# Kernel tuning notes

Measured on AMD Instinct MI355X. Metric: run time of the kernel, lower is better.

The kernel has to match this reference:

```python
import jax, jax.numpy as jnp
import numpy as np

EMBED_DIM = 1024
CONTEXT_LEN = 2048
NUM_HEADS = 16
HEAD_DIM = EMBED_DIM // NUM_HEADS
BATCH = 2
SEQ = 2048


def setup_inputs() -> dict:
    key = jax.random.key(0)
    ks = jax.random.split(key, 6)
    s = 1.0 / np.sqrt(EMBED_DIM)
    x = jax.random.normal(ks[0], (BATCH, SEQ, EMBED_DIM), dtype=jnp.float32)
    # nn.Linear weights stored as [out, in]; we keep [in, out] for x @ W
    W_q = jax.random.uniform(ks[1], (EMBED_DIM, EMBED_DIM), jnp.float32, -s, s)
    W_k = jax.random.uniform(ks[2], (EMBED_DIM, EMBED_DIM), jnp.float32, -s, s)
    W_v = jax.random.uniform(ks[3], (EMBED_DIM, EMBED_DIM), jnp.float32, -s, s)
    W_o = jax.random.uniform(ks[4], (EMBED_DIM, EMBED_DIM), jnp.float32, -s, s)
    b_o = jax.random.uniform(ks[5], (EMBED_DIM,), jnp.float32, -s, s)
    return {"x": x, "W_q": W_q, "W_k": W_k, "W_v": W_v, "W_o": W_o, "b_o": b_o}


def reference(x, W_q, W_k, W_v, W_o, b_o):
    b, s, _ = x.shape
    # project and split heads: [b, s, e] -> [b, h, s, d]
    def heads(t):
        return t.reshape(b, s, NUM_HEADS, HEAD_DIM).transpose(0, 2, 1, 3)
    q = heads(x @ W_q)
    k = heads(x @ W_k)
    v = heads(x @ W_v)
    scores = jnp.einsum("bhqd,bhkd->bhqk", q, k)  # full seq x seq scores
    causal = jnp.triu(jnp.ones((s, s), dtype=bool), k=1)
    scores = jnp.where(causal, -jnp.inf, scores)
    attn = jax.nn.softmax(scores / np.sqrt(HEAD_DIM).astype(np.float32), axis=-1)
    ctx = jnp.einsum("bhqk,bhkd->bhqd", attn, v)
    ctx = ctx.transpose(0, 2, 1, 3).reshape(b, s, EMBED_DIM)
    return ctx @ W_o + b_o
```

## Files before the change

kernel.cpp:

```cpp
#include <hip/hip_runtime.h>

#define EMBED 1024
#define SEQL  2048
#define NHEAD 16
#define HDIM  64
#define NBATCH 2
#define MROWS 4096

typedef __attribute__((ext_vector_type(4))) float  f32x4;
typedef __attribute__((ext_vector_type(8))) __bf16 bf16x8;

__device__ __forceinline__ short f2bf(float f){
  __bf16 h = (__bf16)f;
  union { __bf16 h; short s; } u; u.h = h;
  return u.s;
}

#define GLDS(gp, lp) __builtin_amdgcn_global_load_lds( \
    (const __attribute__((address_space(1))) void*)(gp), \
    (__attribute__((address_space(3))) void*)(lp), 16, 0, 0)

__global__ __launch_bounds__(256) void prep_kernel(const float* __restrict__ x,
    const float* __restrict__ W0, const float* __restrict__ W1,
    const float* __restrict__ W2, const float* __restrict__ W3,
    short* __restrict__ Xb, short* __restrict__ WtAll){
  const int z = blockIdx.z;
  if (z < 4){
    __shared__ float T[64][65];
    const int idx = blockIdx.y*32 + blockIdx.x;
    if (idx >= 256) return;
    const float* W = (z==0)?W0:(z==1)?W1:(z==2)?W2:W3;
    short* Wt = WtAll + z*(EMBED*EMBED);
    const int bx = (idx & 15)*64;
    const int by = (idx >> 4)*64;
    const int c4 = (threadIdx.x & 15)*4;
    const int tr = threadIdx.x >> 4;
    #pragma unroll
    for (int i=0;i<4;++i){
      int r = 16*i + tr;
      float4 v = *(const float4*)(W + (by + r)*EMBED + bx + c4);
      T[c4+0][r] = v.x; T[c4+1][r] = v.y; T[c4+2][r] = v.z; T[c4+3][r] = v.w;
    }
    __syncthreads();
    #pragma unroll
    for (int i=0;i<4;++i){
      int n = 16*i + tr;
      short4 o;
      o.x = f2bf(T[n][c4+0]); o.y = f2bf(T[n][c4+1]);
      o.z = f2bf(T[n][c4+2]); o.w = f2bf(T[n][c4+3]);
      *(short4*)(Wt + (bx + n)*EMBED + by + c4) = o;
    }
  } else {
    const int blk = (z-4)*1024 + blockIdx.y*32 + blockIdx.x;
    const int i = (blk*256 + threadIdx.x)*4;
    float4 v = *(const float4*)(x + i);
    short4 o; o.x=f2bf(v.x); o.y=f2bf(v.y); o.z=f2bf(v.z); o.w=f2bf(v.w);
    *(short4*)(Xb + i) = o;
  }
}

__device__ __forceinline__ void gemm_tile_128(const short* __restrict__ A,
    const short* __restrict__ Bt, short* As, short* Bs, int m0, int n0, f32x4 acc[4][4]){
  const int tid  = threadIdx.x;
  const int lane = tid & 63;
  const int wid  = tid >> 6;
  const int wrow = (wid >> 1) * 64, wcol = (wid & 1) * 64;
  const int arow = tid >> 2, acol8 = (tid & 3) * 8;
  const int l15 = lane & 15, lg = lane >> 4;

  auto STAGE = [&](int b, int k0){
    short* as = As + b*4096;
    short* bs = Bs + b*4096;
    GLDS(A  + (m0      + arow) * 1024 + k0 + acol8, as + tid*8);
    GLDS(A  + (m0 + 64 + arow) * 1024 + k0 + acol8, as + 2048 + tid*8);
    GLDS(Bt + (n0      + arow) * 1024 + k0 + acol8, bs + tid*8);
    GLDS(Bt + (n0 + 64 + arow) * 1024 + k0 + acol8, bs + 2048 + tid*8);
  };

  auto KSTEP = [&](int b){
    const short* as = As + b*4096;
    const short* bs = Bs + b*4096;
    bf16x8 a[4], bb[4];
    #pragma unroll
    for (int i=0;i<4;++i) a[i]  = *(const bf16x8*)(as + (wrow+16*i+l15)*32 + 8*lg);
    #pragma unroll
    for (int j=0;j<4;++j) bb[j] = *(const bf16x8*)(bs + (wcol+16*j+l15)*32 + 8*lg);
    #pragma unroll
    for (int i=0;i<4;++i)
      #pragma unroll
      for (int j=0;j<4;++j)
        acc[i][j] = __builtin_amdgcn_mfma_f32_16x16x32_bf16(a[i], bb[j], acc[i][j], 0,0,0);
  };

  STAGE(0, 0); STAGE(1, 32);
  __syncthreads();
  for (int p = 0; p < 16; ++p){
    const int k0 = p*64;
    if (p + 1 < 16){ STAGE((2*p+2)&3, k0+64); STAGE((2*p+3)&3, k0+96); }
    KSTEP((2*p)&3);
    KSTEP((2*p+1)&3);
    __syncthreads();
  }
}

__device__ __forceinline__ void gemm_tile_64(const short* __restrict__ A,
    const short* __restrict__ Bt, short* As, short* Bs, int m0, int n0, f32x4 acc[2][4]){
  const int tid  = threadIdx.x;
  const int lane = tid & 63;
  const int wid  = tid >> 6;
  const int wrow = (wid >> 1) * 32, wcol = (wid & 1) * 64;
  const int arow = tid >> 2, acol8 = (tid & 3) * 8;
  const int l15 = lane & 15, lg = lane >> 4;

  auto STAGE = [&](int b, int k0){
    short* as = As + b*2048;
    short* bs = Bs + b*4096;
    GLDS(A  + (m0      + arow) * 1024 + k0 + acol8, as + tid*8);
    GLDS(Bt + (n0      + arow) * 1024 + k0 + acol8, bs + tid*8);
    GLDS(Bt + (n0 + 64 + arow) * 1024 + k0 + acol8, bs + 2048 + tid*8);
  };

  auto KSTEP = [&](int b){
    const short* as = As + b*2048;
    const short* bs = Bs + b*4096;
    bf16x8 a[2], bb[4];
    #pragma unroll
    for (int i=0;i<2;++i) a[i]  = *(const bf16x8*)(as + (wrow+16*i+l15)*32 + 8*lg);
    #pragma unroll
    for (int j=0;j<4;++j) bb[j] = *(const bf16x8*)(bs + (wcol+16*j+l15)*32 + 8*lg);
    #pragma unroll
    for (int i=0;i<2;++i)
      #pragma unroll
      for (int j=0;j<4;++j)
        acc[i][j] = __builtin_amdgcn_mfma_f32_16x16x32_bf16(a[i], bb[j], acc[i][j], 0,0,0);
  };

  STAGE(0, 0); STAGE(1, 32);
  __syncthreads();
  for (int p = 0; p < 16; ++p){
    const int k0 = p*64;
    if (p + 1 < 16){ STAGE((2*p+2)&3, k0+64); STAGE((2*p+3)&3, k0+96); }
    KSTEP((2*p)&3);
    KSTEP((2*p+1)&3);
    __syncthreads();
  }
}

__global__ __launch_bounds__(256) void gemm_qkv_kernel(const short* __restrict__ Xb,
    const short* __restrict__ WtAll, short* __restrict__ Q, short* __restrict__ K,
    short* __restrict__ Vt){
  __shared__ __align__(16) short SH[32768];
  short* As = SH;
  short* Bs = SH + 16384;
  const int m0 = blockIdx.x*128, n0 = blockIdx.y*128, z = blockIdx.z;
  const short* Bt = WtAll + z*(EMBED*EMBED);
  f32x4 acc[4][4] = {};
  gemm_tile_128(Xb, Bt, As, Bs, m0, n0, acc);
  const int tid  = threadIdx.x;
  const int lane = tid & 63;
  const int wid  = tid >> 6;
  const int wrow = (wid >> 1) * 64, wcol = (wid & 1) * 64;
  const int l15 = lane & 15, lg = lane >> 4;
  const int bb = m0 >> 11, srow0 = m0 & 2047;

  if (z < 2){
    short* out = z ? K : Q;
    const float qscl = (z==0) ? (0.125f * 1.44269504f) : 1.0f;
    #pragma unroll
    for (int i=0;i<4;++i)
      #pragma unroll
      for (int j=0;j<4;++j)
        #pragma unroll
        for (int r=0;r<4;++r){
          int m = m0 + wrow + 16*i + 4*lg + r;
          int n = n0 + wcol + 16*j + l15;
          int srow = m & 2047, hh = n >> 6, d = n & 63;
          out[(((bb<<4)+hh)*SEQL + srow)*HDIM + d] = f2bf(acc[i][j][r] * qscl);
        }
  } else {
    short* T = SH;
    #pragma unroll
    for (int i=0;i<4;++i)
      #pragma unroll
      for (int j=0;j<4;++j){
        int n_loc = wcol + 16*j + l15;
        int mb    = wrow + 16*i + 4*lg;
        short4 pk;
        pk.x = f2bf(acc[i][j][0]); pk.y = f2bf(acc[i][j][1]);
        pk.z = f2bf(acc[i][j][2]); pk.w = f2bf(acc[i][j][3]);
        *(short4*)(T + n_loc*128 + (mb ^ ((n_loc & 7) << 3))) = pk;
      }
    __syncthreads();
    #pragma unroll
    for (int it=0; it<8; ++it){
      int n_loc = 16*it + (tid >> 4);
      int mch   = (tid & 15) * 8;
      int4 v = *(const int4*)(T + n_loc*128 + (mch ^ ((n_loc & 7) << 3)));
      int n_glob = n0 + n_loc;
      int hh = n_glob >> 6, d = n_glob & 63;
      *(int4*)(Vt + (((bb<<4)+hh)*HDIM + d)*SEQL + srow0 + mch) = v;
    }
  }
}

__global__ __launch_bounds__(256) void gemm_out_kernel(const short* __restrict__ Ctx,
    const short* __restrict__ WtO, const float* __restrict__ bias, float* __restrict__ out){
  __shared__ __align__(16) short As[4*2048], Bs[4*4096];
  const int m0 = blockIdx.x*64, n0 = blockIdx.y*128;
  f32x4 acc[2][4] = {};
  gemm_tile_64(Ctx, WtO, As, Bs, m0, n0, acc);
  const int lane = threadIdx.x & 63;
  const int wid  = threadIdx.x >> 6;
  const int wrow = (wid >> 1) * 32, wcol = (wid & 1) * 64;
  const int l15 = lane & 15, lg = lane >> 4;
  #pragma unroll
  for (int i=0;i<2;++i)
    #pragma unroll
    for (int j=0;j<4;++j)
      #pragma unroll
      for (int r=0;r<4;++r){
        int m = m0 + wrow + 16*i + 4*lg + r;
        int n = n0 + wcol + 16*j + l15;
        out[m*EMBED + n] = acc[i][j][r] + bias[n];
      }
}

__global__ __launch_bounds__(512, 4) void attn_kernel(const short* __restrict__ Q,
    const short* __restrict__ K, const short* __restrict__ Vt, short* __restrict__ Ctx){
  __shared__ __align__(16) char lds[81920];
  const int tid  = threadIdx.x;
  const int lane = tid & 63;
  const int wid  = tid >> 6;
  const int bid   = blockIdx.x;
  const int xcd   = bid & 7;
  const int i7    = bid >> 3;
  const int bh    = xcd + 8*(i7 & 3);
  const int cidx  = i7 >> 2;
  const int chunk = (cidx < 8) ? cidx : 23 - cidx;
  const int q0blk = chunk * 128;
  const int ntp   = chunk + 1;
  const int q0w   = q0blk + 16*wid;
  const int qlast = q0w + 15;

  const short* Qh  = Q  + bh*(SEQL*HDIM);
  const char*  KhB = (const char*)(K  + bh*(SEQL*HDIM));
  const char*  VhB = (const char*)(Vt + bh*(HDIM*SEQL));
  const int l15 = lane & 15, lg = lane >> 4;
  const int lg20 = 20 * lg;
  const int swE = (l15 & 7) << 3;
  const int swB = (l15 & 7) << 4;
  const int laneRow = lane >> 3;
  const int colSwz  = 16 * ((lane & 7) ^ laneRow);
  const int r0 = 8 * wid;

  const short* qp = Qh + (q0w + l15)*HDIM + 8*lg;
  bf16x8 bq0 = *(const bf16x8*)qp;
  bf16x8 bq1 = *(const bf16x8*)(qp + 32);

  f32x4 acc[4];
  #pragma unroll
  for (int j=0; j<4; ++j) acc[j] = (f32x4){0.f,0.f,0.f,0.f};
  float mrun = -3e30f, lrun = 0.f;

  short* pw = (short*)(lds + 65536 + wid*2048);

  auto STAGE = [&](int b, int t){
    char* kb = lds + b*16384;
    char* vb = kb + 8192;
    const int kv0 = t*64;
    GLDS(KhB + (kv0 + r0 + laneRow)*128 + colSwz, kb + r0*128);
    GLDS(VhB + (r0 + laneRow)*4096 + kv0*2 + colSwz, vb + r0*128);
  };

  auto QKHALF = [&](const char* kb, f32x4 sc[4]){
    #pragma unroll
    for (int c=0; c<4; ++c){
      const char* kr = kb + (16*c + l15)*128;
      bf16x8 k0 = *(const bf16x8*)(kr + ((16*lg) ^ swB));
      bf16x8 k1 = *(const bf16x8*)(kr + ((64 + 16*lg) ^ swB));
      f32x4 z = (f32x4){0.f,0.f,0.f,0.f};
      z = __builtin_amdgcn_mfma_f32_16x16x32_bf16(k0, bq0, z, 0,0,0);
      z = __builtin_amdgcn_mfma_f32_16x16x32_bf16(k1, bq1, z, 0,0,0);
      sc[c] = z;
    }
  };

  STAGE(0, 0); STAGE(1, 1);
  __syncthreads();

  for (int tp = 0; tp < ntp; ++tp){
    const int t0   = 2*tp;
    const int kv00 = t0*64;
    const int kv01 = kv00 + 64;
    if (tp + 1 < ntp){ STAGE((t0+2)&3, t0+2); STAGE((t0+3)&3, t0+3); }
    if (kv00 <= qlast){
      const char* kb0 = lds + (t0&3)*16384;
      const char* kb1 = lds + ((t0+1)&3)*16384;
      const bool  h1  = (kv01 <= qlast);
      f32x4 sc0[4], sc1[4];
      __builtin_amdgcn_s_setprio(1);
      QKHALF(kb0, sc0);
      if (h1) QKHALF(kb1, sc1);
      __builtin_amdgcn_s_setprio(0);
      if (kv00 + 63 > q0w){
        #pragma unroll
        for (int c=0; c<4; ++c)
          #pragma unroll
          for (int r=0; r<4; ++r)
            if (kv00 + 16*c + 4*lg + r > q0w + l15) sc0[c][r] = -3e30f;
      }
      if (h1 && kv01 + 63 > q0w){
        #pragma unroll
        for (int c=0; c<4; ++c)
          #pragma unroll
          for (int r=0; r<4; ++r)
            if (kv01 + 16*c + 4*lg + r > q0w + l15) sc1[c][r] = -3e30f;
      }
      float cm[4];
      #pragma unroll
      for (int c=0; c<4; ++c)
        cm[c] = fmaxf(fmaxf(sc0[c][0], sc0[c][1]), fmaxf(sc0[c][2], sc0[c][3]));
      float pm = fmaxf(fmaxf(cm[0], cm[1]), fmaxf(cm[2], cm[3]));
      if (h1){
        float dm[4];
        #pragma unroll
        for (int c=0; c<4; ++c)
          dm[c] = fmaxf(fmaxf(sc1[c][0], sc1[c][1]), fmaxf(sc1[c][2], sc1[c][3]));
        pm = fmaxf(pm, fmaxf(fmaxf(dm[0], dm[1]), fmaxf(dm[2], dm[3])));
      }
      pm = fmaxf(pm, __shfl_xor(pm, 16));
      pm = fmaxf(pm, __shfl_xor(pm, 32));
      const int resc = !__all(pm <= mrun);
      float mn = mrun, ss = 1.0f;
      if (resc){
        mn = fmaxf(mrun, pm);
        ss = __builtin_amdgcn_exp2f(mrun - mn);
        mrun = mn;
      }
      #pragma unroll
      for (int c=0; c<4; ++c)
        #pragma unroll
        for (int r=0; r<4; ++r)
          sc0[c][r] = __builtin_amdgcn_exp2f(sc0[c][r] - mn);
      float cs[4];
      #pragma unroll
      for (int c=0; c<4; ++c)
        cs[c] = (sc0[c][0] + sc0[c][1]) + (sc0[c][2] + sc0[c][3]);
      float ls = (cs[0] + cs[1]) + (cs[2] + cs[3]);
      if (h1){
        #pragma unroll
        for (int c=0; c<4; ++c)
          #pragma unroll
          for (int r=0; r<4; ++r)
            sc1[c][r] = __builtin_amdgcn_exp2f(sc1[c][r] - mn);
        float ds[4];
        #pragma unroll
        for (int c=0; c<4; ++c)
          ds[c] = (sc1[c][0] + sc1[c][1]) + (sc1[c][2] + sc1[c][3]);
        ls += (ds[0] + ds[1]) + (ds[2] + ds[3]);
      }
      ls += __shfl_xor(ls, 16);
      ls += __shfl_xor(ls, 32);
      if (resc){
        lrun = lrun*ss + ls;
        float srg[4];
        #pragma unroll
        for (int r=0; r<4; ++r) srg[r] = __shfl(ss, lg20 + r);
        #pragma unroll
        for (int j=0; j<4; ++j)
          #pragma unroll
          for (int r=0; r<4; ++r) acc[j][r] *= srg[r];
      } else {
        lrun += ls;
      }
      #pragma unroll
      for (int c=0; c<4; ++c){
        short4 pk;
        pk.x = f2bf(sc0[c][0]); pk.y = f2bf(sc0[c][1]);
        pk.z = f2bf(sc0[c][2]); pk.w = f2bf(sc0[c][3]);
        *(short4*)(pw + l15*64 + ((16*c + 4*lg) ^ swE)) = pk;
      }
      {
        bf16x8 pa0 = *(const bf16x8*)(pw + l15*64 + ((8*lg)      ^ swE));
        bf16x8 pa1 = *(const bf16x8*)(pw + l15*64 + ((32 + 8*lg) ^ swE));
        const char* vb = kb0 + 8192;
        __builtin_amdgcn_s_setprio(1);
        #pragma unroll
        for (int j=0; j<4; ++j){
          const char* vrp = vb + (16*j + l15)*128;
          bf16x8 v0 = *(const bf16x8*)(vrp + ((16*lg) ^ swB));
          bf16x8 v1 = *(const bf16x8*)(vrp + ((64 + 16*lg) ^ swB));
          acc[j] = __builtin_amdgcn_mfma_f32_16x16x32_bf16(pa0, v0, acc[j], 0,0,0);
          acc[j] = __builtin_amdgcn_mfma_f32_16x16x32_bf16(pa1, v1, acc[j], 0,0,0);
        }
        __builtin_amdgcn_s_setprio(0);
      }
      if (h1){
        #pragma unroll
        for (int c=0; c<4; ++c){
          short4 pk;
          pk.x = f2bf(sc1[c][0]); pk.y = f2bf(sc1[c][1]);
          pk.z = f2bf(sc1[c][2]); pk.w = f2bf(sc1[c][3]);
          *(short4*)(pw + l15*64 + ((16*c + 4*lg) ^ swE)) = pk;
        }
        bf16x8 pa0 = *(const bf16x8*)(pw + l15*64 + ((8*lg)      ^ swE));
        bf16x8 pa1 = *(const bf16x8*)(pw + l15*64 + ((32 + 8*lg) ^ swE));
        const char* vb = kb1 + 8192;
        __builtin_amdgcn_s_setprio(1);
        #pragma unroll
        for (int j=0; j<4; ++j){
          const char* vrp = vb + (16*j + l15)*128;
          bf16x8 v0 = *(const bf16x8*)(vrp + ((16*lg) ^ swB));
          bf16x8 v1 = *(const bf16x8*)(vrp + ((64 + 16*lg) ^ swB));
          acc[j] = __builtin_amdgcn_mfma_f32_16x16x32_bf16(pa0, v0, acc[j], 0,0,0);
          acc[j] = __builtin_amdgcn_mfma_f32_16x16x32_bf16(pa1, v1, acc[j], 0,0,0);
        }
        __builtin_amdgcn_s_setprio(0);
      }
    }
    __syncthreads();
  }

  const int bb = bh >> 4, hh = bh & 15;
  float lr[4];
  #pragma unroll
  for (int r=0; r<4; ++r) lr[r] = __builtin_amdgcn_rcpf(__shfl(lrun, lg20 + r));
  #pragma unroll
  for (int j=0; j<4; ++j)
    #pragma unroll
    for (int r=0; r<4; ++r){
      int qg = q0w + 4*lg + r;
      Ctx[(bb*SEQL + qg)*EMBED + hh*HDIM + 16*j + l15] = f2bf(acc[j][r] * lr[r]);
    }
}

extern "C" void kernel_launch(void* const* d_in, const int* in_sizes, int n_in,
                              void* d_out, int out_size, void* d_ws, size_t ws_size,
                              hipStream_t stream){
  const float* x  = (const float*)d_in[0];
  const float* Wq = (const float*)d_in[1];
  const float* Wk = (const float*)d_in[2];
  const float* Wv = (const float*)d_in[3];
  const float* Wo = (const float*)d_in[4];
  const float* bo = (const float*)d_in[5];
  float* out = (float*)d_out;

  char* ws = (char*)d_ws;
  const size_t MB = 1u << 20;
  short* Xb  = (short*)(ws +  0*MB);
  short* Wt  = (short*)(ws +  8*MB);
  short* Q   = (short*)(ws + 16*MB);
  short* Kk  = (short*)(ws + 24*MB);
  short* Vt  = (short*)(ws + 32*MB);
  short* Ctx = (short*)(ws + 40*MB);

  prep_kernel<<<dim3(32,32,8), 256, 0, stream>>>(x, Wq, Wk, Wv, Wo, Xb, Wt);
  gemm_qkv_kernel<<<dim3(32,8,3), 256, 0, stream>>>(Xb, Wt, Q, Kk, Vt);
  attn_kernel<<<512, 512, 0, stream>>>(Q, Kk, Vt, Ctx);
  gemm_out_kernel<<<dim3(64,8), 256, 0, stream>>>(Ctx, Wt + 3*(EMBED*EMBED), bo, out);
}
```

Measured before the change: 101.5 us.

## Rewrite QKV GEMM with 256x256 tiles, 8 waves and half-tile pipelined staging

Rebuilds the QKV projection GEMM around 256x256 output tiles per 512-thread block. Operand tiles are staged into swizzled LDS in half-tile pieces, interleaved with four quadrant MFMA phases that use explicit vmcnt waits, barriers and setprio. Larger tiles give more data reuse per LDS load and fewer blocks, and the finer staging is meant to overlap global loads with compute. The cost is only 192 blocks, which may underfill the GPU, plus much higher register and LDS use per block.

```diff
diff --git a/kernel.cpp b/kernel.cpp
--- a/kernel.cpp
+++ b/kernel.cpp
@@ -19,6 +19,11 @@
 #define GLDS(gp, lp) __builtin_amdgcn_global_load_lds( \
     (const __attribute__((address_space(1))) void*)(gp), \
     (__attribute__((address_space(3))) void*)(lp), 16, 0, 0)
+
+#define WAITV(N) do { asm volatile("s_waitcnt vmcnt(" #N ")" ::: "memory"); \
+                      __builtin_amdgcn_sched_barrier(0); } while(0)
+#define BARRIER() do { __builtin_amdgcn_s_barrier(); \
+                       __builtin_amdgcn_sched_barrier(0); } while(0)
 
 __global__ __launch_bounds__(256) void prep_kernel(const float* __restrict__ x,
     const float* __restrict__ W0, const float* __restrict__ W1,
@@ -59,34 +64,158 @@
   }
 }
 
-__device__ __forceinline__ void gemm_tile_128(const short* __restrict__ A,
-    const short* __restrict__ Bt, short* As, short* Bs, int m0, int n0, f32x4 acc[4][4]){
+__global__ __launch_bounds__(512, 2) void gemm_qkv_kernel(const short* __restrict__ Xb,
+    const short* __restrict__ WtAll, short* __restrict__ Q, short* __restrict__ K,
+    short* __restrict__ Vt){
+  __shared__ __align__(16) short SH[65536];
   const int tid  = threadIdx.x;
   const int lane = tid & 63;
   const int wid  = tid >> 6;
-  const int wrow = (wid >> 1) * 64, wcol = (wid & 1) * 64;
+  const int wm   = wid >> 2;
+  const int wn   = wid & 3;
+  const int l15  = lane & 15, lg = lane >> 4;
+  const int swzS = (l15 & 7) << 3;
+  const int m0 = blockIdx.x * 256;
+  const int n0 = blockIdx.y * 256;
+  const int z  = blockIdx.z;
+  const short* A  = Xb;
+  const short* Bt = WtAll + z*(EMBED*EMBED);
+
+  f32x4 acc[8][4] = {};
+
+  auto STAGEH = [&](int mat, int h, int t){
+    const short* src  = mat ? Bt : A;
+    const int   base0 = mat ? n0 : m0;
+    short* dst = SH + (t&1)*32768 + mat*16384 + h*8192;
+    #pragma unroll
+    for (int g=0; g<2; ++g){
+      int c = g*512 + tid;
+      int r = c >> 3;
+      int p = (c & 7) ^ (r & 7);
+      GLDS(src + (base0 + 128*h + r)*1024 + t*64 + p*8, dst + c*8);
+    }
+  };
+
+  auto PH = [&](int t, int qm, int qn){
+    const short* As = SH + (t&1)*32768;
+    const short* Bs = As + 16384;
+    bf16x8 a[4][2], b[2][2];
+    #pragma unroll
+    for (int i=0;i<4;++i){
+      int row = qm*128 + wm*64 + 16*i + l15;
+      #pragma unroll
+      for (int kh=0;kh<2;++kh)
+        a[i][kh] = *(const bf16x8*)(As + row*64 + ((kh*32 + 8*lg) ^ swzS));
+    }
+    #pragma unroll
+    for (int j=0;j<2;++j){
+      int row = qn*128 + wn*32 + 16*j + l15;
+      #pragma unroll
+      for (int kh=0;kh<2;++kh)
+        b[j][kh] = *(const bf16x8*)(Bs + row*64 + ((kh*32 + 8*lg) ^ swzS));
+    }
+    BARRIER();
+    __builtin_amdgcn_s_setprio(1);
+    #pragma unroll
+    for (int i=0;i<4;++i)
+      #pragma unroll
+      for (int j=0;j<2;++j)
+        #pragma unroll
+        for (int kh=0;kh<2;++kh)
+          acc[qm*4+i][qn*2+j] = __builtin_amdgcn_mfma_f32_16x16x32_bf16(
+              a[i][kh], b[j][kh], acc[qm*4+i][qn*2+j], 0,0,0);
+    __builtin_amdgcn_s_setprio(0);
+    WAITV(6);
+    BARRIER();
+  };
+
+  STAGEH(0,0,0); STAGEH(1,0,0); STAGEH(1,1,0); STAGEH(0,1,0);
+  STAGEH(0,0,1); STAGEH(1,0,1);
+  WAITV(4);
+  BARRIER();
+
+  for (int t = 0; t < 16; ++t){
+    if (t+1 < 16) STAGEH(1,1,t+1);
+    PH(t, 0, 0);
+    if (t+1 < 16) STAGEH(0,1,t+1);
+    PH(t, 1, 0);
+    if (t+2 < 16) STAGEH(1,0,t+2);
+    PH(t, 0, 1);
+    if (t+2 < 16) STAGEH(0,0,t+2);
+    PH(t, 1, 1);
+  }
+  WAITV(0);
+  __syncthreads();
+
+  const int bb = m0 >> 11, srow0 = m0 & 2047;
+  if (z < 2){
+    short* out = z ? K : Q;
+    const float qscl = (z==0) ? (0.125f * 1.44269504f) : 1.0f;
+    #pragma unroll
+    for (int mi=0; mi<8; ++mi)
+      #pragma unroll
+      for (int nj=0; nj<4; ++nj)
+        #pragma unroll
+        for (int rr=0; rr<4; ++rr){
+          int m = m0 + 128*(mi>>2) + 64*wm + 16*(mi&3) + 4*lg + rr;
+          int n = n0 + 128*(nj>>1) + 32*wn + 16*(nj&1) + l15;
+          int srow = m & 2047, hh = n >> 6, d = n & 63;
+          out[(((bb<<4)+hh)*SEQL + srow)*HDIM + d] = f2bf(acc[mi][nj][rr] * qscl);
+        }
+  } else {
+    short* T = SH;
+    #pragma unroll
+    for (int mi=0; mi<8; ++mi)
+      #pragma unroll
+      for (int nj=0; nj<4; ++nj){
+        int n_loc = 128*(nj>>1) + 32*wn + 16*(nj&1) + l15;
+        int mb    = 128*(mi>>2) + 64*wm + 16*(mi&3) + 4*lg;
+        short4 pk;
+        pk.x = f2bf(acc[mi][nj][0]); pk.y = f2bf(acc[mi][nj][1]);
+        pk.z = f2bf(acc[mi][nj][2]); pk.w = f2bf(acc[mi][nj][3]);
+        *(short4*)(T + n_loc*256 + (mb ^ ((n_loc & 7) << 3))) = pk;
+      }
+    __syncthreads();
+    #pragma unroll
+    for (int it=0; it<16; ++it){
+      int ci    = it*512 + tid;
+      int n_loc = ci >> 5;
+      int mch   = (ci & 31) * 8;
+      int4 v = *(const int4*)(T + n_loc*256 + (mch ^ ((n_loc & 7) << 3)));
+      int n_glob = n0 + n_loc;
+      int hh = n_glob >> 6, d = n_glob & 63;
+      *(int4*)(Vt + (((bb<<4)+hh)*HDIM + d)*SEQL + srow0 + mch) = v;
+    }
+  }
+}
+
+__device__ __forceinline__ void gemm_tile_64(const short* __restrict__ A,
+    const short* __restrict__ Bt, short* As, short* Bs, int m0, int n0, f32x4 acc[2][4]){
+  const int tid  = threadIdx.x;
+  const int lane = tid & 63;
+  const int wid  = tid >> 6;
+  const int wrow = (wid >> 1) * 32, wcol = (wid & 1) * 64;
   const int arow = tid >> 2, acol8 = (tid & 3) * 8;
   const int l15 = lane & 15, lg = lane >> 4;
 
   auto STAGE = [&](int b, int k0){
-    short* as = As + b*4096;
+    short* as = As + b*2048;
     short* bs = Bs + b*4096;
     GLDS(A  + (m0      + arow) * 1024 + k0 + acol8, as + tid*8);
-    GLDS(A  + (m0 + 64 + arow) * 1024 + k0 + acol8, as + 2048 + tid*8);
     GLDS(Bt + (n0      + arow) * 1024 + k0 + acol8, bs + tid*8);
     GLDS(Bt + (n0 + 64 + arow) * 1024 + k0 + acol8, bs + 2048 + tid*8);
   };
 
   auto KSTEP = [&](int b){
-    const short* as = As + b*4096;
+    const short* as = As + b*2048;
     const short* bs = Bs + b*4096;
-    bf16x8 a[4], bb[4];
-    #pragma unroll
-    for (int i=0;i<4;++i) a[i]  = *(const bf16x8*)(as + (wrow+16*i+l15)*32 + 8*lg);
+    bf16x8 a[2], bb[4];
+    #pragma unroll
+    for (int i=0;i<2;++i) a[i]  = *(const bf16x8*)(as + (wrow+16*i+l15)*32 + 8*lg);
     #pragma unroll
     for (int j=0;j<4;++j) bb[j] = *(const bf16x8*)(bs + (wcol+16*j+l15)*32 + 8*lg);
     #pragma unroll
-    for (int i=0;i<4;++i)
+    for (int i=0;i<2;++i)
       #pragma unroll
       for (int j=0;j<4;++j)
         acc[i][j] = __builtin_amdgcn_mfma_f32_16x16x32_bf16(a[i], bb[j], acc[i][j], 0,0,0);
@@ -100,106 +229,6 @@
     KSTEP((2*p)&3);
     KSTEP((2*p+1)&3);
     __syncthreads();
-  }
-}
-
-__device__ __forceinline__ void gemm_tile_64(const short* __restrict__ A,
-    const short* __restrict__ Bt, short* As, short* Bs, int m0, int n0, f32x4 acc[2][4]){
-  const int tid  = threadIdx.x;
-  const int lane = tid & 63;
-  const int wid  = tid >> 6;
-  const int wrow = (wid >> 1) * 32, wcol = (wid & 1) * 64;
-  const int arow = tid >> 2, acol8 = (tid & 3) * 8;
-  const int l15 = lane & 15, lg = lane >> 4;
-
-  auto STAGE = [&](int b, int k0){
-    short* as = As + b*2048;
-    short* bs = Bs + b*4096;
-    GLDS(A  + (m0      + arow) * 1024 + k0 + acol8, as + tid*8);
-    GLDS(Bt + (n0      + arow) * 1024 + k0 + acol8, bs + tid*8);
-    GLDS(Bt + (n0 + 64 + arow) * 1024 + k0 + acol8, bs + 2048 + tid*8);
-  };
-
-  auto KSTEP = [&](int b){
-    const short* as = As + b*2048;
-    const short* bs = Bs + b*4096;
-    bf16x8 a[2], bb[4];
-    #pragma unroll
-    for (int i=0;i<2;++i) a[i]  = *(const bf16x8*)(as + (wrow+16*i+l15)*32 + 8*lg);
-    #pragma unroll
-    for (int j=0;j<4;++j) bb[j] = *(const bf16x8*)(bs + (wcol+16*j+l15)*32 + 8*lg);
-    #pragma unroll
-    for (int i=0;i<2;++i)
-      #pragma unroll
-      for (int j=0;j<4;++j)
-        acc[i][j] = __builtin_amdgcn_mfma_f32_16x16x32_bf16(a[i], bb[j], acc[i][j], 0,0,0);
-  };
-
-  STAGE(0, 0); STAGE(1, 32);
-  __syncthreads();
-  for (int p = 0; p < 16; ++p){
-    const int k0 = p*64;
-    if (p + 1 < 16){ STAGE((2*p+2)&3, k0+64); STAGE((2*p+3)&3, k0+96); }
-    KSTEP((2*p)&3);
-    KSTEP((2*p+1)&3);
-    __syncthreads();
-  }
-}
-
-__global__ __launch_bounds__(256) void gemm_qkv_kernel(const short* __restrict__ Xb,
-    const short* __restrict__ WtAll, short* __restrict__ Q, short* __restrict__ K,
-    short* __restrict__ Vt){
-  __shared__ __align__(16) short SH[32768];
-  short* As = SH;
-  short* Bs = SH + 16384;
-  const int m0 = blockIdx.x*128, n0 = blockIdx.y*128, z = blockIdx.z;
-  const short* Bt = WtAll + z*(EMBED*EMBED);
-  f32x4 acc[4][4] = {};
-  gemm_tile_128(Xb, Bt, As, Bs, m0, n0, acc);
-  const int tid  = threadIdx.x;
-  const int lane = tid & 63;
-  const int wid  = tid >> 6;
-  const int wrow = (wid >> 1) * 64, wcol = (wid & 1) * 64;
-  const int l15 = lane & 15, lg = lane >> 4;
-  const int bb = m0 >> 11, srow0 = m0 & 2047;
-
-  if (z < 2){
-    short* out = z ? K : Q;
-    const float qscl = (z==0) ? (0.125f * 1.44269504f) : 1.0f;
-    #pragma unroll
-    for (int i=0;i<4;++i)
-      #pragma unroll
-      for (int j=0;j<4;++j)
-        #pragma unroll
-        for (int r=0;r<4;++r){
-          int m = m0 + wrow + 16*i + 4*lg + r;
-          int n = n0 + wcol + 16*j + l15;
-          int srow = m & 2047, hh = n >> 6, d = n & 63;
-          out[(((bb<<4)+hh)*SEQL + srow)*HDIM + d] = f2bf(acc[i][j][r] * qscl);
-        }
-  } else {
-    short* T = SH;
-    #pragma unroll
-    for (int i=0;i<4;++i)
-      #pragma unroll
-      for (int j=0;j<4;++j){
-        int n_loc = wcol + 16*j + l15;
-        int mb    = wrow + 16*i + 4*lg;
-        short4 pk;
-        pk.x = f2bf(acc[i][j][0]); pk.y = f2bf(acc[i][j][1]);
-        pk.z = f2bf(acc[i][j][2]); pk.w = f2bf(acc[i][j][3]);
-        *(short4*)(T + n_loc*128 + (mb ^ ((n_loc & 7) << 3))) = pk;
-      }
-    __syncthreads();
-    #pragma unroll
-    for (int it=0; it<8; ++it){
-      int n_loc = 16*it + (tid >> 4);
-      int mch   = (tid & 15) * 8;
-      int4 v = *(const int4*)(T + n_loc*128 + (mch ^ ((n_loc & 7) << 3)));
-      int n_glob = n0 + n_loc;
-      int hh = n_glob >> 6, d = n_glob & 63;
-      *(int4*)(Vt + (((bb<<4)+hh)*HDIM + d)*SEQL + srow0 + mch) = v;
-    }
   }
 }
 
@@ -278,10 +307,10 @@
       const char* kr = kb + (16*c + l15)*128;
       bf16x8 k0 = *(const bf16x8*)(kr + ((16*lg) ^ swB));
       bf16x8 k1 = *(const bf16x8*)(kr + ((64 + 16*lg) ^ swB));
-      f32x4 z = (f32x4){0.f,0.f,0.f,0.f};
-      z = __builtin_amdgcn_mfma_f32_16x16x32_bf16(k0, bq0, z, 0,0,0);
-      z = __builtin_amdgcn_mfma_f32_16x16x32_bf16(k1, bq1, z, 0,0,0);
-      sc[c] = z;
+      f32x4 zz = (f32x4){0.f,0.f,0.f,0.f};
+      zz = __builtin_amdgcn_mfma_f32_16x16x32_bf16(k0, bq0, zz, 0,0,0);
+      zz = __builtin_amdgcn_mfma_f32_16x16x32_bf16(k1, bq1, zz, 0,0,0);
+      sc[c] = zz;
     }
   };
 
@@ -455,7 +484,7 @@
   short* Ctx = (short*)(ws + 40*MB);
 
   prep_kernel<<<dim3(32,32,8), 256, 0, stream>>>(x, Wq, Wk, Wv, Wo, Xb, Wt);
-  gemm_qkv_kernel<<<dim3(32,8,3), 256, 0, stream>>>(Xb, Wt, Q, Kk, Vt);
+  gemm_qkv_kernel<<<dim3(16,4,3), 512, 0, stream>>>(Xb, Wt, Q, Kk, Vt);
   attn_kernel<<<512, 512, 0, stream>>>(Q, Kk, Vt, Ctx);
   gemm_out_kernel<<<dim3(64,8), 256, 0, stream>>>(Ctx, Wt + 3*(EMBED*EMBED), bo, out);
 }
```

New measurement: 104.2 us. 2.7% more time.
